# Performance work log

Measured on AMD Instinct MI355X. Metric: run time of the kernel, lower is better.

## Reference

```python
import jax, jax.numpy as jnp
import numpy as np

D_MODEL = 768
N_HEAD = 12
D_FF = 3072
EPS = 1e-5


def _layer_norm(x, w, b):
    mu = jnp.mean(x, axis=-1, keepdims=True)
    var = jnp.mean(jnp.square(x - mu), axis=-1, keepdims=True)
    return (x - mu) * jax.lax.rsqrt(var + EPS) * w + b


def setup_inputs() -> dict:
    key = jax.random.key(0)
    ks = jax.random.split(key, 8)
    B, S, D = 2, 4096, D_MODEL
    s_in = 1.0 / np.sqrt(D)
    s_ff = 1.0 / np.sqrt(D_FF)
    return {
        "src": jax.random.normal(ks[0], (B, S, D), jnp.float32),
        "w_qkv": jax.random.uniform(ks[1], (3 * D, D), jnp.float32, -s_in, s_in),
        "b_qkv": jnp.zeros((3 * D,), jnp.float32),
        "w_out": jax.random.uniform(ks[2], (D, D), jnp.float32, -s_in, s_in),
        "b_out": jnp.zeros((D,), jnp.float32),
        "w1": jax.random.uniform(ks[3], (D_FF, D), jnp.float32, -s_in, s_in),
        "b1": jnp.zeros((D_FF,), jnp.float32),
        "w2": jax.random.uniform(ks[4], (D, D_FF), jnp.float32, -s_ff, s_ff),
        "b2": jnp.zeros((D,), jnp.float32),
        "ln1_w": jnp.ones((D,), jnp.float32),
        "ln1_b": jnp.zeros((D,), jnp.float32),
        "ln2_w": jnp.ones((D,), jnp.float32),
        "ln2_b": jnp.zeros((D,), jnp.float32),
    }


def reference(src, w_qkv, b_qkv, w_out, b_out, w1, b1, w2, b2,
              ln1_w, ln1_b, ln2_w, ln2_b):
    B, S, D = src.shape
    H, dh = N_HEAD, D // N_HEAD
    # fused QKV projection: [B,S,3D]
    qkv = jnp.einsum('bsd,ed->bse', src, w_qkv) + b_qkv
    q, k, v = jnp.split(qkv, 3, axis=-1)
    q = q.reshape(B, S, H, dh)
    k = k.reshape(B, S, H, dh)
    v = v.reshape(B, S, H, dh)
    scale = 1.0 / np.sqrt(dh)
    scores = jnp.einsum('bqhd,bkhd->bhqk', q, k) * scale  # [B,H,S,S]
    attn = jax.nn.softmax(scores, axis=-1)
    ctx = jnp.einsum('bhqk,bkhd->bqhd', attn, v).reshape(B, S, D)
    attn_out = jnp.einsum('bsd,ed->bse', ctx, w_out) + b_out
    # post-norm residual (norm_first=False), dropout inactive in eval
    x = _layer_norm(src + attn_out, ln1_w, ln1_b)
    h = jax.nn.relu(jnp.einsum('bsd,fd->bsf', x, w1) + b1)
    ffn = jnp.einsum('bsf,df->bsd', h, w2) + b2
    return _layer_norm(x + ffn, ln2_w, ln2_b)
```

## Files before the change

### kernel.cpp

```cpp
#include <hip/hip_runtime.h>
#include <hip/hip_bf16.h>

typedef __hip_bfloat16 bf16;
typedef __attribute__((ext_vector_type(8))) short s16x8;
typedef __attribute__((ext_vector_type(4))) float f32x4;

#define MFMA16x16x32(A, B, C) __builtin_amdgcn_mfma_f32_16x16x32_bf16((A), (B), (C), 0, 0, 0)

__device__ __forceinline__ void async_copy16(const bf16* g, bf16* l) {
  __builtin_amdgcn_global_load_lds(
      (const __attribute__((address_space(1))) void*)g,
      (__attribute__((address_space(3))) void*)l, 16, 0, 0);
}

__device__ __forceinline__ int SW(int row, int chunk) {
  return row * 64 + (((chunk) ^ (row & 7)) << 3);
}

__global__ __launch_bounds__(256)
void cast_all_kernel(const float* __restrict__ s0, bf16* __restrict__ d0,
                     const float* __restrict__ s1, bf16* __restrict__ d1,
                     const float* __restrict__ s2, bf16* __restrict__ d2,
                     const float* __restrict__ s3, bf16* __restrict__ d3,
                     const float* __restrict__ s4, bf16* __restrict__ d4) {
  int blk = blockIdx.x;
  const float* in; bf16* out;
  if (blk < 1728)      { in = s0; out = d0; }
  else if (blk < 2304) { in = s1; out = d1; blk -= 1728; }
  else if (blk < 4608) { in = s2; out = d2; blk -= 2304; }
  else if (blk < 6912) { in = s3; out = d3; blk -= 4608; }
  else                 { in = s4; out = d4; blk -= 6912; }
  const int i = (blk * 256 + threadIdx.x) * 4;
  const float4 f = *(const float4*)(in + i);
  out[i + 0] = (bf16)f.x; out[i + 1] = (bf16)f.y;
  out[i + 2] = (bf16)f.z; out[i + 3] = (bf16)f.w;
}

template <int RELU, int VT, int ACCUM, int CN, typename OutT>
__global__ __launch_bounds__(256)
void gemm_bt_kernel(const bf16* __restrict__ A, const bf16* __restrict__ B,
                    const float* __restrict__ bias, OutT* __restrict__ C,
                    int N, int K, int lda, int ldb, bf16* __restrict__ C2) {
  constexpr int NJ = CN / 32;
  __shared__ __align__(16) bf16 As[2][128 * 32];
  __shared__ __align__(16) bf16 Bs[2][CN * 32];

  const int t = threadIdx.x;
  const int lane = t & 63;
  const int wave = t >> 6;
  const int wm = (wave >> 1) << 6;
  const int wn = (wave & 1) * (CN / 2);
  const int col16 = lane & 15;
  const int quad = lane >> 4;
  const int bm = blockIdx.x;
  const int bn = blockIdx.y;

  const bf16* Ag = A + (size_t)(bm * 128 + (t >> 2)) * lda + (t & 3) * 8;
  const bf16* Bg = B + (size_t)(bn * CN + (t >> 2)) * ldb + (t & 3) * 8;

  f32x4 acc[4][NJ] = {};

  async_copy16(Ag, &As[0][0] + t * 8);
  async_copy16(Ag + (size_t)64 * lda, &As[0][0] + 2048 + t * 8);
  async_copy16(Bg, &Bs[0][0] + t * 8);
  if (CN == 128)
    async_copy16(Bg + (size_t)64 * ldb, &Bs[0][0] + 2048 + t * 8);

  int n = 0;
  for (int k0 = 0; k0 < K; k0 += 32, n ^= 1) {
    __syncthreads();
    if (k0 + 32 < K) {
      const int k1 = k0 + 32;
      async_copy16(Ag + k1, &As[n ^ 1][0] + t * 8);
      async_copy16(Ag + (size_t)64 * lda + k1, &As[n ^ 1][0] + 2048 + t * 8);
      async_copy16(Bg + k1, &Bs[n ^ 1][0] + t * 8);
      if (CN == 128)
        async_copy16(Bg + (size_t)64 * ldb + k1, &Bs[n ^ 1][0] + 2048 + t * 8);
    }
    const bf16* asn = &As[n][0];
    const bf16* bsn = &Bs[n][0];

    s16x8 af[4], bfr[NJ];
#pragma unroll
    for (int i = 0; i < 4; i++)
      af[i] = *(const s16x8*)(asn + (wm + i * 16 + col16) * 32 + quad * 8);
#pragma unroll
    for (int j = 0; j < NJ; j++)
      bfr[j] = *(const s16x8*)(bsn + (wn + j * 16 + col16) * 32 + quad * 8);
#pragma unroll
    for (int i = 0; i < 4; i++)
#pragma unroll
      for (int j = 0; j < NJ; j++)
        acc[i][j] = MFMA16x16x32(af[i], bfr[j], acc[i][j]);
  }

  const int row0 = bm * 128 + wm + quad * 4;
  const int col0 = bn * CN + wn + col16;
#pragma unroll
  for (int j = 0; j < NJ; j++) {
    const int col = col0 + j * 16;
    const float bv = ACCUM ? 0.0f : bias[col];
#pragma unroll
    for (int i = 0; i < 4; i++) {
#pragma unroll
      for (int r = 0; r < 4; r++) {
        float v = acc[i][j][r] + bv;
        if (RELU) v = fmaxf(v, 0.0f);
        const int row = row0 + i * 16 + r;
        if (VT == 2) {
          if (col < 1536) {
            C[(size_t)row * N + col] = (OutT)v;
          } else {
            const int cc = col - 1536;
            C2[(size_t)((row >> 12) * 12 + (cc >> 6)) * 262144 +
               (cc & 63) * 4096 + (row & 4095)] = (bf16)v;
          }
        } else {
          const size_t idx = (size_t)row * N + col;
          if (ACCUM) v += ((const float*)C)[idx];
          C[idx] = (OutT)v;
        }
      }
    }
  }
}

__global__ __launch_bounds__(256, 2)
void attn_kernel(const bf16* __restrict__ QK, const bf16* __restrict__ Vt,
                 bf16* __restrict__ Opart, float* __restrict__ lbuf) {
  __shared__ __align__(16) bf16 Ks[2][64 * 64];
  __shared__ __align__(16) bf16 Vs[2][64 * 64];
  __shared__ __align__(16) bf16 Ps[4][64 * 64];

  const int t = threadIdx.x, lane = t & 63, wave = t >> 6;
  const int col16 = lane & 15, quad = lane >> 4;
  const int b = blockIdx.z, h = blockIdx.y;
  const int ks = blockIdx.x >> 4;
  const int qblk = blockIdx.x & 15;
  const int qw0 = qblk * 256 + wave * 64;

  s16x8 bq[4][2];
#pragma unroll
  for (int qt = 0; qt < 4; qt++)
#pragma unroll
    for (int s = 0; s < 2; s++) {
      union { s16x8 v; bf16 hh[8]; } u;
      u.v = *(const s16x8*)(QK + (size_t)(b * 4096 + qw0 + qt * 16 + col16) * 1536 +
                            h * 64 + s * 32 + quad * 8);
#pragma unroll
      for (int e = 0; e < 8; e++) u.hh[e] = (bf16)((float)u.hh[e] * 0.18033688f);
      bq[qt][s] = u.v;
    }

  union { s16x8 v; short s_[8]; } uo1;
#pragma unroll
  for (int e = 0; e < 8; e++) uo1.s_[e] = (short)0x3F80;
  const s16x8 aones = uo1.v;

  const int srow = t >> 3;
  const int schx = (t & 7) ^ (srow & 7);
  const bf16* kgb = QK + (size_t)(b * 4096) * 1536 + 768 + h * 64;
  const bf16* vgb = Vt + (size_t)(b * 12 + h) * 262144;
  const bf16* ksrc0 = kgb + (size_t)srow * 1536 + schx * 8;
  const bf16* ksrc1 = kgb + (size_t)(32 + srow) * 1536 + schx * 8;
  const bf16* vsrc0 = vgb + (size_t)srow * 4096 + schx * 8;
  const bf16* vsrc1 = vgb + (size_t)(32 + srow) * 4096 + schx * 8;

  f32x4 o[4][4] = {};
  f32x4 lacc[4] = {};
  bf16* pw = &Ps[wave][0];

  const int kbeg = ks * 2048, kend = kbeg + 2048;

  async_copy16(ksrc0 + (size_t)kbeg * 1536, &Ks[0][0] + t * 8);
  async_copy16(ksrc1 + (size_t)kbeg * 1536, &Ks[0][0] + 2048 + t * 8);
  async_copy16(vsrc0 + kbeg, &Vs[0][0] + t * 8);
  async_copy16(vsrc1 + kbeg, &Vs[0][0] + 2048 + t * 8);

  int n = 0;
  for (int k0 = kbeg; k0 < kend; k0 += 64, n ^= 1) {
    __syncthreads();
    if (k0 + 64 < kend) {
      const int k1 = k0 + 64;
      async_copy16(ksrc0 + (size_t)k1 * 1536, &Ks[n ^ 1][0] + t * 8);
      async_copy16(ksrc1 + (size_t)k1 * 1536, &Ks[n ^ 1][0] + 2048 + t * 8);
      async_copy16(vsrc0 + k1, &Vs[n ^ 1][0] + t * 8);
      async_copy16(vsrc1 + k1, &Vs[n ^ 1][0] + 2048 + t * 8);
    }
    const bf16* ksn = &Ks[n][0];
    const bf16* vsn = &Vs[n][0];

    s16x8 ak[2][4];
#pragma unroll
    for (int s = 0; s < 2; s++)
#pragma unroll
      for (int kt = 0; kt < 4; kt++)
        ak[s][kt] = *(const s16x8*)(ksn + SW(kt * 16 + col16, s * 4 + quad));

#pragma unroll
    for (int kt = 0; kt < 4; kt++) {
      f32x4 st[4] = {};
#pragma unroll
      for (int s = 0; s < 2; s++)
#pragma unroll
        for (int qt = 0; qt < 4; qt++)
          st[qt] = MFMA16x16x32(ak[s][kt], bq[qt][s], st[qt]);
#pragma unroll
      for (int qt = 0; qt < 4; qt++) {
        union { unsigned long long u; bf16 hh[4]; } pk;
#pragma unroll
        for (int r = 0; r < 4; r++)
          pk.hh[r] = (bf16)__builtin_amdgcn_exp2f(st[qt][r]);
        *(unsigned long long*)(pw + (qt * 16 + col16) * 64 +
                               (((kt * 2 + (quad >> 1)) ^ (col16 & 7)) << 3) +
                               (quad & 1) * 4) = pk.u;
      }
    }
    asm volatile("s_waitcnt lgkmcnt(0)" ::: "memory");

#pragma unroll
    for (int s = 0; s < 2; s++) {
      s16x8 bp[4];
#pragma unroll
      for (int qt = 0; qt < 4; qt++)
        bp[qt] = *(const s16x8*)(pw + SW(qt * 16 + col16, s * 4 + quad));
#pragma unroll
      for (int qt = 0; qt < 4; qt++)
        lacc[qt] = MFMA16x16x32(aones, bp[qt], lacc[qt]);
#pragma unroll
      for (int dt = 0; dt < 4; dt++) {
        const s16x8 av = *(const s16x8*)(vsn + SW(dt * 16 + col16, s * 4 + quad));
#pragma unroll
        for (int qt = 0; qt < 4; qt++)
          o[dt][qt] = MFMA16x16x32(av, bp[qt], o[dt][qt]);
      }
    }
  }

  if (lane < 16) {
#pragma unroll
    for (int qt = 0; qt < 4; qt++)
      lbuf[(size_t)ks * 98304 + (size_t)(b * 4096 + qw0 + qt * 16 + lane) * 12 + h] =
          lacc[qt][0];
  }

#pragma unroll
  for (int qt = 0; qt < 4; qt++)
#pragma unroll
    for (int dt = 0; dt < 4; dt++)
#pragma unroll
      for (int r = 0; r < 4; r++)
        pw[(qt * 16 + col16) * 64 + (((dt * 2 + (quad >> 1)) ^ (col16 & 7)) << 3) +
           (quad & 1) * 4 + r] = (bf16)(o[dt][qt][r]);
  asm volatile("s_waitcnt lgkmcnt(0)" ::: "memory");
  const int qrow = lane >> 1, chalf = (lane & 1) * 4;
#pragma unroll
  for (int h2 = 0; h2 < 2; h2++) {
    const int rl = h2 * 32 + qrow;
    bf16* dst = Opart + (size_t)ks * 6291456 +
                (size_t)(b * 4096 + qw0 + rl) * 768 + h * 64 + chalf * 8;
#pragma unroll
    for (int i = 0; i < 4; i++)
      *(s16x8*)(dst + i * 8) = *(const s16x8*)(pw + SW(rl, chalf + i));
  }
}

__global__ __launch_bounds__(256)
void attn_combine_kernel(const bf16* __restrict__ Opart,
                         const float* __restrict__ lbuf,
                         bf16* __restrict__ ctx) {
  const int i = blockIdx.x * 256 + threadIdx.x;
  const int row = i / 96, c8 = i % 96;
  const int h = c8 >> 3;
  const float inv = 1.0f / (lbuf[(size_t)row * 12 + h] +
                            lbuf[98304 + (size_t)row * 12 + h]);
  union { s16x8 v; bf16 hh[8]; } ua, ub, uo;
  ua.v = *(const s16x8*)(Opart + (size_t)row * 768 + c8 * 8);
  ub.v = *(const s16x8*)(Opart + 6291456 + (size_t)row * 768 + c8 * 8);
#pragma unroll
  for (int j = 0; j < 8; j++)
    uo.hh[j] = (bf16)(((float)ua.hh[j] + (float)ub.hh[j]) * inv);
  *(s16x8*)(ctx + (size_t)row * 768 + c8 * 8) = uo.v;
}

__global__ __launch_bounds__(256)
void add_ln_b_kernel(const float* __restrict__ X, const float* __restrict__ Y,
                     const float* __restrict__ w, const float* __restrict__ b,
                     bf16* __restrict__ out) {
  const int row = blockIdx.x * 4 + (threadIdx.x >> 6);
  const int lane = threadIdx.x & 63;
  const float* x = X + (size_t)row * 768;
  const float* y = Y + (size_t)row * 768;
  float v[12];
  float s = 0.0f;
#pragma unroll
  for (int i = 0; i < 3; i++) {
    const int c = lane * 4 + i * 256;
    const float4 xf = *(const float4*)(x + c);
    const float4 yf = *(const float4*)(y + c);
    v[i * 4 + 0] = xf.x + yf.x; v[i * 4 + 1] = xf.y + yf.y;
    v[i * 4 + 2] = xf.z + yf.z; v[i * 4 + 3] = xf.w + yf.w;
    s += v[i * 4] + v[i * 4 + 1] + v[i * 4 + 2] + v[i * 4 + 3];
  }
#pragma unroll
  for (int off = 32; off > 0; off >>= 1) s += __shfl_xor(s, off, 64);
  const float mu = s * (1.0f / 768.0f);
  float var = 0.0f;
#pragma unroll
  for (int i = 0; i < 12; i++) { const float d = v[i] - mu; var += d * d; }
#pragma unroll
  for (int off = 32; off > 0; off >>= 1) var += __shfl_xor(var, off, 64);
  const float rs = rsqrtf(var * (1.0f / 768.0f) + 1e-5f);
#pragma unroll
  for (int i = 0; i < 12; i++) {
    const int c = lane * 4 + (i >> 2) * 256 + (i & 3);
    out[(size_t)row * 768 + c] = (bf16)((v[i] - mu) * rs * w[c] + b[c]);
  }
}

__global__ __launch_bounds__(256)
void add_ln_f_kernel(const bf16* __restrict__ X, const float* __restrict__ Y,
                     const float* __restrict__ w, const float* __restrict__ b,
                     float* __restrict__ out) {
  const int row = blockIdx.x * 4 + (threadIdx.x >> 6);
  const int lane = threadIdx.x & 63;
  const bf16* x = X + (size_t)row * 768;
  const float* y = Y + (size_t)row * 768;
  float v[12];
  float s = 0.0f;
#pragma unroll
  for (int i = 0; i < 3; i++) {
    const int c = lane * 4 + i * 256;
    const float4 yf = *(const float4*)(y + c);
    v[i * 4 + 0] = (float)x[c + 0] + yf.x; v[i * 4 + 1] = (float)x[c + 1] + yf.y;
    v[i * 4 + 2] = (float)x[c + 2] + yf.z; v[i * 4 + 3] = (float)x[c + 3] + yf.w;
    s += v[i * 4] + v[i * 4 + 1] + v[i * 4 + 2] + v[i * 4 + 3];
  }
#pragma unroll
  for (int off = 32; off > 0; off >>= 1) s += __shfl_xor(s, off, 64);
  const float mu = s * (1.0f / 768.0f);
  float var = 0.0f;
#pragma unroll
  for (int i = 0; i < 12; i++) { const float d = v[i] - mu; var += d * d; }
#pragma unroll
  for (int off = 32; off > 0; off >>= 1) var += __shfl_xor(var, off, 64);
  const float rs = rsqrtf(var * (1.0f / 768.0f) + 1e-5f);
#pragma unroll
  for (int i = 0; i < 12; i++) {
    const int c = lane * 4 + (i >> 2) * 256 + (i & 3);
    out[(size_t)row * 768 + c] = (v[i] - mu) * rs * w[c] + b[c];
  }
}

extern "C" void kernel_launch(void* const* d_in, const int* in_sizes, int n_in,
                              void* d_out, int out_size, void* d_ws, size_t ws_size,
                              hipStream_t stream) {
  (void)in_sizes; (void)n_in; (void)out_size; (void)ws_size;
  const float* src   = (const float*)d_in[0];
  const float* w_qkv = (const float*)d_in[1];
  const float* b_qkv = (const float*)d_in[2];
  const float* w_out = (const float*)d_in[3];
  const float* b_out = (const float*)d_in[4];
  const float* w1    = (const float*)d_in[5];
  const float* b1    = (const float*)d_in[6];
  const float* w2    = (const float*)d_in[7];
  const float* b2    = (const float*)d_in[8];
  const float* ln1w  = (const float*)d_in[9];
  const float* ln1b  = (const float*)d_in[10];
  const float* ln2w  = (const float*)d_in[11];
  const float* ln2b  = (const float*)d_in[12];
  float* out = (float*)d_out;

  char* ws = (char*)d_ws;
  bf16* wqkvb = (bf16*)ws;
  bf16* woutb = (bf16*)(ws + 3538944);
  bf16* w1b   = (bf16*)(ws + 4718592);
  bf16* w2b   = (bf16*)(ws + 9437184);
  bf16* srcb  = (bf16*)(ws + 14155776);
  bf16* QK    = (bf16*)(ws + 26738688);
  bf16* Vt    = (bf16*)(ws + 51904512);
  bf16* Opart = (bf16*)d_out;
  float* lbuf = (float*)ws;
  bf16* ctx   = (bf16*)(ws + 14155776);
  float* attn_out = (float*)(ws + 26738688);
  bf16* x1b   = (bf16*)(ws + 51904512);
  bf16* hbuf  = (bf16*)(ws + 14155776);
  float* ffn  = out;

  cast_all_kernel<<<13056, 256, 0, stream>>>(
      w_qkv, wqkvb, w_out, woutb, w1, w1b, w2, w2b, src, srcb);

  gemm_bt_kernel<0, 2, 0, 128, bf16><<<dim3(64, 18), 256, 0, stream>>>(
      srcb, wqkvb, b_qkv, QK, 1536, 768, 768, 768, Vt);
  attn_kernel<<<dim3(32, 12, 2), 256, 0, stream>>>(QK, Vt, Opart, lbuf);
  attn_combine_kernel<<<3072, 256, 0, stream>>>(Opart, lbuf, ctx);
  gemm_bt_kernel<0, 0, 0, 64, float><<<dim3(64, 12), 256, 0, stream>>>(
      ctx, woutb, b_out, attn_out, 768, 768, 768, 768, nullptr);
  add_ln_b_kernel<<<2048, 256, 0, stream>>>(src, attn_out, ln1w, ln1b, x1b);
  for (int c = 0; c < 2; c++) {
    gemm_bt_kernel<1, 0, 0, 128, bf16><<<dim3(64, 12), 256, 0, stream>>>(
        x1b, w1b + (size_t)c * 1536 * 768, b1 + c * 1536, hbuf, 1536, 768, 768,
        768, nullptr);
    if (c == 0)
      gemm_bt_kernel<0, 0, 0, 64, float><<<dim3(64, 12), 256, 0, stream>>>(
          hbuf, w2b + c * 1536, b2, ffn, 768, 1536, 1536, 3072, nullptr);
    else
      gemm_bt_kernel<0, 0, 1, 64, float><<<dim3(64, 12), 256, 0, stream>>>(
          hbuf, w2b + c * 1536, b2, ffn, 768, 1536, 1536, 3072, nullptr);
  }
  add_ln_f_kernel<<<2048, 256, 0, stream>>>(x1b, ffn, ln2w, ln2b, out);
}
```

Baseline: 459.2 us.

## Triple-buffer attention K/V tiles in 32-key steps with vmcnt waits

Restructures the attention main loop to process 32 keys per step using a three-slot ring buffer of K/V tiles in one shared pool. Explicit vmcnt waits and a bare s_barrier replace __syncthreads, so two tiles stay in flight. The P tile is stored in a padded 40-column layout to cut LDS size, and the occupancy hint in launch_bounds is dropped. This costs more barriers per key and smaller MFMA batches per step, and relies on the hand-written vmcnt counts being correct.

```diff
diff --git a/kernel.cpp b/kernel.cpp
--- a/kernel.cpp
+++ b/kernel.cpp
@@ -125,12 +125,10 @@
   }
 }
 
-__global__ __launch_bounds__(256, 2)
+__global__ __launch_bounds__(256)
 void attn_kernel(const bf16* __restrict__ QK, const bf16* __restrict__ Vt,
                  bf16* __restrict__ Opart, float* __restrict__ lbuf) {
-  __shared__ __align__(16) bf16 Ks[2][64 * 64];
-  __shared__ __align__(16) bf16 Vs[2][64 * 64];
-  __shared__ __align__(16) bf16 Ps[4][64 * 64];
+  __shared__ __align__(16) bf16 pool[22528];
 
   const int t = threadIdx.x, lane = t & 63, wave = t >> 6;
   const int col16 = lane & 15, quad = lane >> 4;
@@ -157,48 +155,53 @@
   for (int e = 0; e < 8; e++) uo1.s_[e] = (short)0x3F80;
   const s16x8 aones = uo1.v;
 
-  const int srow = t >> 3;
-  const int schx = (t & 7) ^ (srow & 7);
+  const int krow = t >> 3;
+  const int kch = (t & 7) ^ (krow & 7);
+  const int vrow = t >> 2;
+  const int vch = (t & 3) ^ ((vrow >> 1) & 3);
   const bf16* kgb = QK + (size_t)(b * 4096) * 1536 + 768 + h * 64;
   const bf16* vgb = Vt + (size_t)(b * 12 + h) * 262144;
-  const bf16* ksrc0 = kgb + (size_t)srow * 1536 + schx * 8;
-  const bf16* ksrc1 = kgb + (size_t)(32 + srow) * 1536 + schx * 8;
-  const bf16* vsrc0 = vgb + (size_t)srow * 4096 + schx * 8;
-  const bf16* vsrc1 = vgb + (size_t)(32 + srow) * 4096 + schx * 8;
+  const bf16* ksrc = kgb + (size_t)krow * 1536 + kch * 8;
+  const bf16* vsrc = vgb + (size_t)vrow * 4096 + vch * 8;
 
   f32x4 o[4][4] = {};
   f32x4 lacc[4] = {};
-  bf16* pw = &Ps[wave][0];
+  bf16* pw = pool + 12288 + wave * 2560;
 
   const int kbeg = ks * 2048, kend = kbeg + 2048;
 
-  async_copy16(ksrc0 + (size_t)kbeg * 1536, &Ks[0][0] + t * 8);
-  async_copy16(ksrc1 + (size_t)kbeg * 1536, &Ks[0][0] + 2048 + t * 8);
-  async_copy16(vsrc0 + kbeg, &Vs[0][0] + t * 8);
-  async_copy16(vsrc1 + kbeg, &Vs[0][0] + 2048 + t * 8);
-
-  int n = 0;
-  for (int k0 = kbeg; k0 < kend; k0 += 64, n ^= 1) {
-    __syncthreads();
+  async_copy16(ksrc + (size_t)kbeg * 1536, pool + t * 8);
+  async_copy16(vsrc + kbeg, pool + 6144 + t * 8);
+  async_copy16(ksrc + (size_t)(kbeg + 32) * 1536, pool + 2048 + t * 8);
+  async_copy16(vsrc + kbeg + 32, pool + 6144 + 2048 + t * 8);
+
+  int ib = 0;
+  for (int k0 = kbeg; k0 < kend; k0 += 32) {
+    const int ip = (ib + 2 >= 3) ? ib - 1 : ib + 2;
     if (k0 + 64 < kend) {
-      const int k1 = k0 + 64;
-      async_copy16(ksrc0 + (size_t)k1 * 1536, &Ks[n ^ 1][0] + t * 8);
-      async_copy16(ksrc1 + (size_t)k1 * 1536, &Ks[n ^ 1][0] + 2048 + t * 8);
-      async_copy16(vsrc0 + k1, &Vs[n ^ 1][0] + t * 8);
-      async_copy16(vsrc1 + k1, &Vs[n ^ 1][0] + 2048 + t * 8);
-    }
-    const bf16* ksn = &Ks[n][0];
-    const bf16* vsn = &Vs[n][0];
-
-    s16x8 ak[2][4];
+      async_copy16(ksrc + (size_t)(k0 + 64) * 1536, pool + ip * 2048 + t * 8);
+      async_copy16(vsrc + k0 + 64, pool + 6144 + ip * 2048 + t * 8);
+      asm volatile("s_waitcnt vmcnt(4)" ::: "memory");
+    } else if (k0 + 32 < kend) {
+      asm volatile("s_waitcnt vmcnt(2)" ::: "memory");
+    } else {
+      asm volatile("s_waitcnt vmcnt(0)" ::: "memory");
+    }
+    __builtin_amdgcn_s_barrier();
+    __builtin_amdgcn_sched_barrier(0);
+
+    const bf16* ksn = pool + ib * 2048;
+    const bf16* vsn = pool + 6144 + ib * 2048;
+
+    s16x8 ak[2][2];
 #pragma unroll
     for (int s = 0; s < 2; s++)
 #pragma unroll
-      for (int kt = 0; kt < 4; kt++)
+      for (int kt = 0; kt < 2; kt++)
         ak[s][kt] = *(const s16x8*)(ksn + SW(kt * 16 + col16, s * 4 + quad));
 
 #pragma unroll
-    for (int kt = 0; kt < 4; kt++) {
+    for (int kt = 0; kt < 2; kt++) {
       f32x4 st[4] = {};
 #pragma unroll
       for (int s = 0; s < 2; s++)
@@ -211,30 +214,30 @@
 #pragma unroll
         for (int r = 0; r < 4; r++)
           pk.hh[r] = (bf16)__builtin_amdgcn_exp2f(st[qt][r]);
-        *(unsigned long long*)(pw + (qt * 16 + col16) * 64 +
-                               (((kt * 2 + (quad >> 1)) ^ (col16 & 7)) << 3) +
-                               (quad & 1) * 4) = pk.u;
+        *(unsigned long long*)(pw + (qt * 16 + col16) * 40 + kt * 16 + quad * 4) =
+            pk.u;
       }
     }
     asm volatile("s_waitcnt lgkmcnt(0)" ::: "memory");
 
-#pragma unroll
-    for (int s = 0; s < 2; s++) {
-      s16x8 bp[4];
+    s16x8 bp[4];
+#pragma unroll
+    for (int qt = 0; qt < 4; qt++)
+      bp[qt] = *(const s16x8*)(pw + (qt * 16 + col16) * 40 + quad * 8);
+#pragma unroll
+    for (int qt = 0; qt < 4; qt++)
+      lacc[qt] = MFMA16x16x32(aones, bp[qt], lacc[qt]);
+#pragma unroll
+    for (int dt = 0; dt < 4; dt++) {
+      const int vr = dt * 16 + col16;
+      const s16x8 av = *(const s16x8*)(vsn + vr * 32 +
+                                       ((quad ^ ((vr >> 1) & 3)) << 3));
 #pragma unroll
       for (int qt = 0; qt < 4; qt++)
-        bp[qt] = *(const s16x8*)(pw + SW(qt * 16 + col16, s * 4 + quad));
-#pragma unroll
-      for (int qt = 0; qt < 4; qt++)
-        lacc[qt] = MFMA16x16x32(aones, bp[qt], lacc[qt]);
-#pragma unroll
-      for (int dt = 0; dt < 4; dt++) {
-        const s16x8 av = *(const s16x8*)(vsn + SW(dt * 16 + col16, s * 4 + quad));
-#pragma unroll
-        for (int qt = 0; qt < 4; qt++)
-          o[dt][qt] = MFMA16x16x32(av, bp[qt], o[dt][qt]);
-      }
-    }
+        o[dt][qt] = MFMA16x16x32(av, bp[qt], o[dt][qt]);
+    }
+
+    ib = (ib + 1 == 3) ? 0 : ib + 1;
   }
 
   if (lane < 16) {
@@ -244,13 +247,15 @@
           lacc[qt][0];
   }
 
+  __syncthreads();
+  bf16* ep = pool + wave * 4096;
 #pragma unroll
   for (int qt = 0; qt < 4; qt++)
 #pragma unroll
     for (int dt = 0; dt < 4; dt++)
 #pragma unroll
       for (int r = 0; r < 4; r++)
-        pw[(qt * 16 + col16) * 64 + (((dt * 2 + (quad >> 1)) ^ (col16 & 7)) << 3) +
+        ep[(qt * 16 + col16) * 64 + (((dt * 2 + (quad >> 1)) ^ (col16 & 7)) << 3) +
            (quad & 1) * 4 + r] = (bf16)(o[dt][qt][r]);
   asm volatile("s_waitcnt lgkmcnt(0)" ::: "memory");
   const int qrow = lane >> 1, chalf = (lane & 1) * 4;
@@ -261,7 +266,7 @@
                 (size_t)(b * 4096 + qw0 + rl) * 768 + h * 64 + chalf * 8;
 #pragma unroll
     for (int i = 0; i < 4; i++)
-      *(s16x8*)(dst + i * 8) = *(const s16x8*)(pw + SW(rl, chalf + i));
+      *(s16x8*)(dst + i * 8) = *(const s16x8*)(ep + SW(rl, chalf + i));
   }
 }
 
```

New measurement: 470.1 us. 1.02x slower.
